# Optimization experiments

Hardware: AMD Instinct MI355X
Metric: run time of the kernel (lower is better)

The kernel has to match this reference:

```python
import jax, jax.numpy as jnp
import numpy as np

N, E, B = 16384, 131072, 256
F_IN, HID, HEADS, F_CELL, N_OUT = 78, 128, 10, 954, 2
NEG_SLOPE = 0.2  # PyG GATConv default


def setup_inputs() -> dict:
    key = jax.random.key(0)
    ks = jax.random.split(key, 24)
    rn = lambda k, shape, s=0.05: (jax.random.normal(k, shape, jnp.float32) * s)
    inp = {
        "x": rn(ks[0], (N, F_IN), 1.0),
        "edge_index": jax.random.randint(ks[1], (2, E), 0, N, dtype=jnp.int32),
        "batch": (jnp.arange(N, dtype=jnp.int32) // (N // B)),  # 64 nodes per graph, sorted
        "cell": rn(ks[2], (B, F_CELL), 1.0),
        "W1": rn(ks[3], (F_IN, HEADS * HID)),
        "a_src1": rn(ks[4], (HEADS, HID)),
        "a_dst1": rn(ks[5], (HEADS, HID)),
        "b1": jnp.zeros((HEADS * HID,), jnp.float32),
        # GATConv layer 2: 1280 -> 128, 1 head
        "W2": rn(ks[6], (HEADS * HID, HID)),
        "a_src2": rn(ks[7], (1, HID)),
        "a_dst2": rn(ks[8], (1, HID)),
        "b2": jnp.zeros((HID,), jnp.float32),
        # drug1_fc_g1: 128 -> 128
        "Wg": rn(ks[9], (HID, HID)), "bg": jnp.zeros((HID,), jnp.float32),
        # fc head applied to normalized cell (source applies fc1 to cell: 954 -> 2048)
        "Wf1": rn(ks[10], (F_CELL, 2048)), "bf1": jnp.zeros((2048,), jnp.float32),
        "Wf2": rn(ks[11], (2048, 512)), "bf2": jnp.zeros((512,), jnp.float32),
        "Wf3": rn(ks[12], (512, 128)), "bf3": jnp.zeros((128,), jnp.float32),
        "Wo": rn(ks[13], (128, N_OUT)), "bo": jnp.zeros((N_OUT,), jnp.float32),
    }
    return inp


def _gat_layer(xin, src, dst, W, a_s, a_d, b, heads, ch):
    """PyG GATConv: linear -> per-edge leaky_relu(a_src.h_j + a_dst.h_i) ->
    segment softmax over incoming edges of dst -> scatter-add of alpha * h_src."""
    n = xin.shape[0]
    h = (xin @ W).reshape(n, heads, ch)                       # [N,H,C]
    es = jnp.einsum('nhc,hc->nh', h, a_s)                     # alpha_src per node
    ed = jnp.einsum('nhc,hc->nh', h, a_d)                     # alpha_dst per node
    e = jax.nn.leaky_relu(es[src] + ed[dst], NEG_SLOPE)       # [Etot,H]
    m = jax.ops.segment_max(e, dst, num_segments=n)           # stable softmax max
    w = jnp.exp(e - m[dst])                                   # unnormalized alpha
    denom = jax.ops.segment_sum(w, dst, num_segments=n)       # [N,H]
    num = jax.ops.segment_sum(w[:, :, None] * h[src], dst, num_segments=n)  # [N,H,C]
    out = num / denom[:, :, None]
    return out.reshape(n, heads * ch) + b


def reference(x, edge_index, batch, cell, W1, a_src1, a_dst1, b1,
              W2, a_src2, a_dst2, b2, Wg, bg, Wf1, bf1, Wf2, bf2,
              Wf3, bf3, Wo, bo):
    n = x.shape[0]
    # add self-loops (PyG GATConv default)
    loop = jnp.arange(n, dtype=edge_index.dtype)
    src = jnp.concatenate([edge_index[0], loop])
    dst = jnp.concatenate([edge_index[1], loop])

    x1 = jax.nn.elu(_gat_layer(x, src, dst, W1, a_src1, a_dst1, b1, HEADS, HID))
    x1 = jax.nn.elu(_gat_layer(x1, src, dst, W2, a_src2, a_dst2, b2, 1, HID))
    # global max pool over graphs (batch is sorted, all B segments non-empty)
    x1 = jax.ops.segment_max(x1, batch, num_segments=B)       # [B,128]
    x1 = jax.nn.relu(x1 @ Wg + bg)

    # cell branch: L2 normalize rows, then dense head (dropout = identity in eval)
    celln = cell / jnp.maximum(jnp.linalg.norm(cell, axis=1, keepdims=True), 1e-12)
    xc = jax.nn.relu(celln @ Wf1 + bf1)
    xc = jax.nn.relu(xc @ Wf2 + bf2)
    xc = jax.nn.relu(xc @ Wf3 + bf3)
    out = xc @ Wo + bo                                        # [B,2]
    # source returns only `out`; we also expose the (otherwise-dead) GAT branch
    return jnp.concatenate([x1, out], axis=1)                 # [B,130]
```

## Files before the change

### kernel.cpp

```cpp
#include <hip/hip_runtime.h>
#include <hip/hip_bf16.h>
#include <math.h>

#define N_NODES 16384
#define E_EDGES 131072
#define ETOT (E_EDGES + N_NODES)
#define BGRAPH 256
#define F_INPUT 78
#define KPAD1 96
#define HID 128
#define HEADS 10
#define F1 (HEADS * HID)
#define F_CELL 954
#define KPADC 960
#define NEG_SLOPE 0.2f

typedef __attribute__((ext_vector_type(8))) short frag_t;
typedef __attribute__((ext_vector_type(4))) float f4_t;

static __device__ __forceinline__ unsigned fkey(float f) {
    unsigned b = __float_as_uint(f);
    return (b & 0x80000000u) ? ~b : (b | 0x80000000u);
}
static __device__ __forceinline__ float funkey(unsigned k) {
    unsigned b = (k & 0x80000000u) ? (k ^ 0x80000000u) : ~k;
    return __uint_as_float(b);
}
static __device__ __forceinline__ unsigned short f2bf(float f) {
    __hip_bfloat16 h = __float2bfloat16(f);
    return *(unsigned short*)&h;
}
static __device__ __forceinline__ float bf2f(unsigned short u) {
    return __uint_as_float(((unsigned)u) << 16);
}

template<int WM16, int WN16, int OUT_MODE, int ACT, int HAS_BIAS>
__global__ __launch_bounds__(256) void mfma_gemm(
    const unsigned short* __restrict__ A, const unsigned short* __restrict__ BT,
    const float* __restrict__ bias, void* __restrict__ C,
    float* __restrict__ esp, float* __restrict__ edp,
    const float* __restrict__ ca, const float* __restrict__ cd,
    int M, int N, int Kpad, int lda, int ldb, int ldc,
    int za, int zb, int zc, int zbias)
{
    constexpr int BM = 32 * WM16, BN = 32 * WN16;
    __shared__ __align__(16) unsigned short Als[BM * 32];
    __shared__ __align__(16) unsigned short Bls[BN * 32];
    const int z = blockIdx.z;
    A  += (size_t)z * za;
    BT += (size_t)z * zb;
    const int t = threadIdx.x;
    const int wave = t >> 6, lane = t & 63;
    const int wr = (wave >> 1) * (16 * WM16);
    const int wc = (wave & 1) * (16 * WN16);
    const int row0 = blockIdx.y * BM;
    const int col0 = blockIdx.x * BN;

    f4_t acc[WM16][WN16];
#pragma unroll
    for (int m = 0; m < WM16; m++)
#pragma unroll
        for (int n = 0; n < WN16; n++) { acc[m][n] = (f4_t){0.f, 0.f, 0.f, 0.f}; }

    const int lrow = lane & 15, kg = lane >> 4;
    for (int kk = 0; kk < Kpad; kk += 32) {
        for (int i = t; i < BM * 4; i += 256) {
            int r = i >> 2, slot = i & 3;
            uint4 v = *(const uint4*)&A[(size_t)(row0 + r) * lda + kk + slot * 8];
            *(uint4*)&Als[r * 32 + ((slot ^ (r & 3) ^ ((r >> 2) & 3)) * 8)] = v;
        }
        for (int i = t; i < BN * 4; i += 256) {
            int r = i >> 2, slot = i & 3;
            uint4 v = *(const uint4*)&BT[(size_t)(col0 + r) * ldb + kk + slot * 8];
            *(uint4*)&Bls[r * 32 + ((slot ^ (r & 3) ^ ((r >> 2) & 3)) * 8)] = v;
        }
        __syncthreads();
        frag_t af[WM16], bfr[WN16];
#pragma unroll
        for (int m = 0; m < WM16; m++) {
            int r = wr + m * 16 + lrow;
            af[m] = *(frag_t*)&Als[r * 32 + ((kg ^ (r & 3) ^ ((r >> 2) & 3)) * 8)];
        }
#pragma unroll
        for (int n = 0; n < WN16; n++) {
            int r = wc + n * 16 + lrow;
            bfr[n] = *(frag_t*)&Bls[r * 32 + ((kg ^ (r & 3) ^ ((r >> 2) & 3)) * 8)];
        }
#pragma unroll
        for (int m = 0; m < WM16; m++)
#pragma unroll
            for (int n = 0; n < WN16; n++)
                acc[m][n] = __builtin_amdgcn_mfma_f32_16x16x32_bf16(af[m], bfr[n], acc[m][n], 0, 0, 0);
        __syncthreads();
    }

    if constexpr (OUT_MODE <= 2 || OUT_MODE == 5) {
#pragma unroll
        for (int m = 0; m < WM16; m++) {
#pragma unroll
            for (int n = 0; n < WN16; n++) {
                int col = col0 + wc + n * 16 + lrow;
                float bv = HAS_BIAS ? bias[z * zbias + col] : 0.f;
#pragma unroll
                for (int r = 0; r < 4; r++) {
                    int row = row0 + wr + m * 16 + kg * 4 + r;
                    float v = acc[m][n][r] + bv;
                    if (ACT == 1) v = fmaxf(v, 0.f);
                    if (ACT == 2) v = (v > 0.f) ? v : expm1f(v);
                    size_t ci = (size_t)row * ldc + (size_t)z * zc + col;
                    if (OUT_MODE == 0)      ((float*)C)[ci] = v;
                    else if (OUT_MODE == 1) ((unsigned short*)C)[ci] = f2bf(v);
                    else if (OUT_MODE == 5) atomicAdd(&((float*)C)[(size_t)row * ldc + col], acc[m][n][r]);
                    else {
                        if (col < 10)                  esp[row * 10 + col] = v;
                        else if (col >= 16 && col < 26) edp[row * 10 + (col - 16)] = v;
                    }
                }
            }
        }
    } else {
        __shared__ float o2l[BM][2];
        if (t < BM) { o2l[t][0] = 0.f; o2l[t][1] = 0.f; }
        __syncthreads();
#pragma unroll
        for (int m = 0; m < WM16; m++) {
#pragma unroll
            for (int r = 0; r < 4; r++) {
                int lr = wr + m * 16 + kg * 4 + r;
                float p0 = 0.f, p1 = 0.f;
#pragma unroll
                for (int n = 0; n < WN16; n++) {
                    int col = col0 + wc + n * 16 + lrow;
                    float v = acc[m][n][r] + (HAS_BIAS ? bias[col] : 0.f);
                    if (ACT == 1) v = fmaxf(v, 0.f);
                    p0 = fmaf(v, ca[col * 2], p0);
                    p1 = fmaf(v, ca[col * 2 + 1], p1);
                }
                atomicAdd(&o2l[lr][0], p0);
                atomicAdd(&o2l[lr][1], p1);
            }
        }
        __syncthreads();
        if (t < BM) {
            ((float*)C)[(size_t)(row0 + t) * ldc + 128] = o2l[t][0] + cd[0];
            ((float*)C)[(size_t)(row0 + t) * ldc + 129] = o2l[t][1] + cd[1];
        }
    }
}

#define S0 1572864
#define S1 122880
#define S2 163840
#define S3 1966080
#define S4 1048576
#define S5 65536
#define S6 16384
#define PREP_TOTAL (S0+S1+S2+S3+S4+S5+S6)
#define NB_ELEM (PREP_TOTAL / 256)
#define NB_FOLD 768
#define NB_ZCNT 64
#define NB_ZPK  128
#define NB_ZH2F 8192

__global__ void prep_all(const float* __restrict__ x,  const float* __restrict__ W1,
                         const float* __restrict__ W2, const float* __restrict__ Wf1,
                         const float* __restrict__ Wf2, const float* __restrict__ Wf3,
                         const float* __restrict__ Wg,
                         const float* __restrict__ as1, const float* __restrict__ ad1,
                         unsigned short* __restrict__ xb,  unsigned short* __restrict__ W1T,
                         unsigned short* __restrict__ W2T, unsigned short* __restrict__ Wf1T,
                         unsigned short* __restrict__ Wf2T, unsigned short* __restrict__ Wf3T,
                         unsigned short* __restrict__ WgT, unsigned short* __restrict__ F1T,
                         int* __restrict__ counts, unsigned* __restrict__ pk,
                         float* __restrict__ H2f)
{
    int blk = blockIdx.x, t = threadIdx.x;
    if (blk < NB_ELEM) {
        int i = blk * 256 + t;
        if (i < S0) { int r = i / 96, k = i % 96;
            xb[i] = (k < F_INPUT) ? f2bf(x[r * F_INPUT + k]) : 0; return; }
        i -= S0;
        if (i < S1) { int n = i / 96, k = i % 96;
            W1T[i] = (k < F_INPUT) ? f2bf(W1[(size_t)k * F1 + n]) : 0; return; }
        i -= S1;
        if (i < S2) { int n = i / 1280, k = i % 1280;
            W2T[i] = f2bf(W2[(size_t)k * HID + n]); return; }
        i -= S2;
        if (i < S3) { int n = i / 960, k = i % 960;
            Wf1T[i] = (k < F_CELL) ? f2bf(Wf1[(size_t)k * 2048 + n]) : 0; return; }
        i -= S3;
        if (i < S4) { int n = i / 2048, k = i % 2048;
            Wf2T[i] = f2bf(Wf2[(size_t)k * 512 + n]); return; }
        i -= S4;
        if (i < S5) { int n = i / 512, k = i % 512;
            Wf3T[i] = f2bf(Wf3[(size_t)k * HID + n]); return; }
        i -= S5;
        { int n = i / 128, k = i % 128;
            WgT[i] = f2bf(Wg[(size_t)k * HID + n]); }
        return;
    }
    blk -= NB_ELEM;
    if (blk < NB_FOLD) {
        int idx = blk * 4 + (t >> 6);
        int l = t & 63;
        int r = idx / 96, k = idx % 96;
        int sd = r >> 4, h = r & 15;
        float p = 0.f;
        if (h < HEADS && k < F_INPUT) {
            const float* a = (sd ? ad1 : as1) + h * HID;
            float2 wv = *(const float2*)&W1[(size_t)k * F1 + h * HID + 2 * l];
            float2 av = *(const float2*)&a[2 * l];
            p = wv.x * av.x + wv.y * av.y;
#pragma unroll
            for (int o = 32; o > 0; o >>= 1) p += __shfl_xor(p, o);
        }
        if (l == 0) F1T[(size_t)r * 96 + k] = f2bf(p);
        return;
    }
    blk -= NB_FOLD;
    if (blk < NB_ZCNT) { counts[blk * 256 + t] = 0; return; }
    blk -= NB_ZCNT;
    if (blk < NB_ZPK) { pk[blk * 256 + t] = 0; return; }
    blk -= NB_ZPK;
    H2f[(size_t)blk * 256 + t] = 0.f;
}

__global__ void hist_dst(const int* __restrict__ ei, int* __restrict__ counts)
{
    int e = blockIdx.x * blockDim.x + threadIdx.x;
    if (e >= ETOT) return;
    int dst = (e < E_EDGES) ? ei[E_EDGES + e] : (e - E_EDGES);
    atomicAdd(&counts[dst], 1);
}

__global__ void scan_counts(const int* __restrict__ counts,
                            int* __restrict__ row_start, int* __restrict__ cursor)
{
    __shared__ int part[256];
    int t = threadIdx.x;
    int base = t * 64;
    int sum = 0;
    for (int i = 0; i < 64; i++) sum += counts[base + i];
    part[t] = sum;
    __syncthreads();
    for (int o = 1; o < 256; o <<= 1) {
        int v = 0;
        if (t >= o) v = part[t - o];
        __syncthreads();
        part[t] += v;
        __syncthreads();
    }
    int run = (t == 0) ? 0 : part[t - 1];
    for (int i = 0; i < 64; i++) {
        row_start[base + i] = run;
        cursor[base + i] = run;
        run += counts[base + i];
    }
    if (t == 255) row_start[N_NODES] = run;
}

__global__ void scatter_csr(const int* __restrict__ ei, int* __restrict__ cursor,
                            int* __restrict__ csr_src)
{
    int e = blockIdx.x * blockDim.x + threadIdx.x;
    if (e >= ETOT) return;
    int src, dst;
    if (e < E_EDGES) { src = ei[e]; dst = ei[E_EDGES + e]; } else { src = dst = e - E_EDGES; }
    int pos = atomicAdd(&cursor[dst], 1);
    csr_src[pos] = src;
}

__global__ __launch_bounds__(256) void h2_convert(
    const float* __restrict__ H2f, const float* __restrict__ as_,
    const float* __restrict__ ad_, unsigned short* __restrict__ H2,
    float* __restrict__ es, float* __restrict__ ed)
{
    int n = blockIdx.x * 4 + (threadIdx.x >> 6);
    int l = threadIdx.x & 63;
    float2 v = *(const float2*)&H2f[(size_t)n * HID + 2 * l];
    float2 av = *(const float2*)&as_[2 * l];
    float2 dv = *(const float2*)&ad_[2 * l];
    float vs = v.x * av.x + v.y * av.y;
    float vd = v.x * dv.x + v.y * dv.y;
#pragma unroll
    for (int o = 32; o > 0; o >>= 1) { vs += __shfl_xor(vs, o); vd += __shfl_xor(vd, o); }
    if (l == 0) { es[n] = vs; ed[n] = vd; }
    unsigned pw = (unsigned)f2bf(v.x) | ((unsigned)f2bf(v.y) << 16);
    *(unsigned*)&H2[(size_t)n * HID + 2 * l] = pw;
}

__global__ __launch_bounds__(256) void gat1_agg(
    const int* __restrict__ row_start, const int* __restrict__ csr_src,
    const unsigned* __restrict__ xb32,
    const float* __restrict__ es, const float* __restrict__ ed,
    unsigned* __restrict__ aggb)
{
    const int w = threadIdx.x >> 6, l = threadIdx.x & 63;
    const int n = blockIdx.x * 4 + w;
    const int rs = row_start[n];
    const int deg = row_start[n + 1] - rs;

    __shared__ __align__(16) float w_lds[4][64][12];
    __shared__ int src_lds[4][64];

    float edv[HEADS];
    const float* edp = ed + n * HEADS;
#pragma unroll
    for (int h = 0; h < HEADS; h++) edv[h] = edp[h];

    float acc0[HEADS], acc1[HEADS], den[HEADS];
#pragma unroll
    for (int h = 0; h < HEADS; h++) { acc0[h] = 0.f; acc1[h] = 0.f; den[h] = 0.f; }

    for (int base = 0; base < deg; base += 64) {
        int e = base + l;
        int cnt = min(64, deg - base);
        float wv[HEADS];
        if (e < deg) {
            int s = csr_src[rs + e];
            src_lds[w][l] = s;
            const float* ep = es + s * HEADS;
#pragma unroll
            for (int h = 0; h < HEADS; h++) {
                float v = ep[h] + edv[h];
                v = (v >= 0.f) ? v : NEG_SLOPE * v;
                wv[h] = __expf(v);
            }
        } else {
#pragma unroll
            for (int h = 0; h < HEADS; h++) wv[h] = 0.f;
        }
#pragma unroll
        for (int h = 0; h < HEADS; h++) {
            den[h] += wv[h];
            w_lds[w][l][h] = wv[h];
        }
        asm volatile("" ::: "memory");

        for (int j = 0; j < cnt; j++) {
            int sj = src_lds[w][j];
            unsigned xv = 0;
            if (l < 48) xv = xb32[(size_t)sj * 48 + l];
            float x0 = bf2f((unsigned short)(xv & 0xffffu));
            float x1v = bf2f((unsigned short)(xv >> 16));
            float4 wa = *(const float4*)&w_lds[w][j][0];
            float4 wb = *(const float4*)&w_lds[w][j][4];
            float2 wcv = *(const float2*)&w_lds[w][j][8];
            float ww[HEADS] = {wa.x, wa.y, wa.z, wa.w, wb.x, wb.y, wb.z, wb.w, wcv.x, wcv.y};
#pragma unroll
            for (int h = 0; h < HEADS; h++) {
                acc0[h] = fmaf(ww[h], x0, acc0[h]);
                acc1[h] = fmaf(ww[h], x1v, acc1[h]);
            }
        }
        asm volatile("" ::: "memory");
    }

#pragma unroll
    for (int h = 0; h < HEADS; h++)
#pragma unroll
        for (int o = 32; o > 0; o >>= 1) den[h] += __shfl_xor(den[h], o);

    if (l < 48) {
        unsigned* orow = aggb + (size_t)n * 480;
#pragma unroll
        for (int h = 0; h < HEADS; h++) {
            float inv = 1.f / den[h];
            unsigned lo = f2bf(acc0[h] * inv);
            unsigned hi = f2bf(acc1[h] * inv);
            orow[h * 48 + l] = lo | (hi << 16);
        }
    }
}

__global__ __launch_bounds__(256) void gat2_agg(
    const int* __restrict__ row_start, const int* __restrict__ csr_src,
    const unsigned short* __restrict__ H2,
    const float* __restrict__ es, const float* __restrict__ ed,
    const float* __restrict__ b, const int* __restrict__ batch,
    unsigned* __restrict__ pk)
{
    const int w = threadIdx.x >> 6, l = threadIdx.x & 63;
    const int n = blockIdx.x * 4 + w;
    const int rs = row_start[n];
    const int deg = row_start[n + 1] - rs;
    const float edv = ed[n];

    float2 acc = {0.f, 0.f};
    float den = 0.f;
    for (int base = 0; base < deg; base += 64) {
        int e = base + l;
        int cnt = min(64, deg - base);
        int s = 0;
        float wv = 0.f;
        if (e < deg) {
            s = csr_src[rs + e];
            float v = es[s] + edv;
            v = (v >= 0.f) ? v : NEG_SLOPE * v;
            wv = __expf(v);
        }
        den += wv;
        for (int j = 0; j < cnt; j++) {
            float wj = __shfl(wv, j);
            int   sj = __shfl(s, j);
            unsigned hp = *(const unsigned*)&H2[(size_t)sj * HID + 2 * l];
            acc.x = fmaf(wj, bf2f((unsigned short)(hp & 0xffffu)), acc.x);
            acc.y = fmaf(wj, bf2f((unsigned short)(hp >> 16)), acc.y);
        }
    }
#pragma unroll
    for (int o = 32; o > 0; o >>= 1) den += __shfl_xor(den, o);

    float inv = 1.f / den;
    float2 bv = *(const float2*)&b[2 * l];
    float v0 = acc.x * inv + bv.x;
    float v1 = acc.y * inv + bv.y;
    v0 = (v0 > 0.f) ? v0 : expm1f(v0);
    v1 = (v1 > 0.f) ? v1 : expm1f(v1);
    int g = batch[n];
    atomicMax(&pk[g * HID + 2 * l], fkey(v0));
    atomicMax(&pk[g * HID + 2 * l + 1], fkey(v1));
}

__global__ void decode_cell(const unsigned* __restrict__ pk,
                            unsigned short* __restrict__ pooledb,
                            const float* __restrict__ cell,
                            unsigned short* __restrict__ celln)
{
    int t = threadIdx.x;
    if (blockIdx.x < BGRAPH) {
        int b = blockIdx.x;
        __shared__ float red[256];
        float s = 0.f;
        for (int c = t; c < F_CELL; c += 256) { float v = cell[(size_t)b * F_CELL + c]; s += v * v; }
        red[t] = s; __syncthreads();
        for (int o = 128; o > 0; o >>= 1) { if (t < o) red[t] += red[t + o]; __syncthreads(); }
        float inv = 1.f / fmaxf(sqrtf(red[0]), 1e-12f);
        for (int c = t; c < KPADC; c += 256) {
            float v = (c < F_CELL) ? cell[(size_t)b * F_CELL + c] * inv : 0.f;
            celln[(size_t)b * KPADC + c] = f2bf(v);
        }
    } else {
        int i = (blockIdx.x - BGRAPH) * 256 + t;
        if (i < BGRAPH * HID) pooledb[i] = f2bf(funkey(pk[i]));
    }
}

extern "C" void kernel_launch(void* const* d_in, const int* in_sizes, int n_in,
                              void* d_out, int out_size, void* d_ws, size_t ws_size,
                              hipStream_t stream)
{
    const float* x    = (const float*)d_in[0];
    const int*   ei   = (const int*)d_in[1];
    const int*   batch= (const int*)d_in[2];
    const float* cell = (const float*)d_in[3];
    const float* W1   = (const float*)d_in[4];
    const float* as1  = (const float*)d_in[5];
    const float* ad1  = (const float*)d_in[6];
    const float* b1   = (const float*)d_in[7];
    const float* W2   = (const float*)d_in[8];
    const float* as2  = (const float*)d_in[9];
    const float* ad2  = (const float*)d_in[10];
    const float* b2   = (const float*)d_in[11];
    const float* Wg   = (const float*)d_in[12];
    const float* bg   = (const float*)d_in[13];
    const float* Wf1  = (const float*)d_in[14];
    const float* bf1  = (const float*)d_in[15];
    const float* Wf2  = (const float*)d_in[16];
    const float* bf2  = (const float*)d_in[17];
    const float* Wf3  = (const float*)d_in[18];
    const float* bf3  = (const float*)d_in[19];
    const float* Wo   = (const float*)d_in[20];
    const float* bo   = (const float*)d_in[21];
    float* out = (float*)d_out;

    char* w = (char*)d_ws;
    auto alloc = [&](size_t bytes) { char* p = w; w += (bytes + 255) & ~(size_t)255; return p; };
    unsigned short* xb   = (unsigned short*)alloc((size_t)N_NODES * KPAD1 * 2);
    unsigned short* W1T  = (unsigned short*)alloc((size_t)F1 * KPAD1 * 2);
    unsigned short* F1T  = (unsigned short*)alloc((size_t)32 * KPAD1 * 2);
    unsigned*       aggb = (unsigned*)alloc((size_t)N_NODES * 480 * 4);
    unsigned short* x1   = (unsigned short*)alloc((size_t)N_NODES * F1 * 2);
    unsigned short* W2T  = (unsigned short*)alloc((size_t)HID * F1 * 2);
    float*          H2f  = (float*)alloc((size_t)N_NODES * HID * 4);
    unsigned short* H2   = (unsigned short*)alloc((size_t)N_NODES * HID * 2);
    float*    es1  = (float*)alloc((size_t)N_NODES * HEADS * 4);
    float*    ed1  = (float*)alloc((size_t)N_NODES * HEADS * 4);
    float*    es2  = (float*)alloc((size_t)N_NODES * 4);
    float*    ed2  = (float*)alloc((size_t)N_NODES * 4);
    int*      counts    = (int*)alloc((size_t)N_NODES * 4);
    int*      row_start = (int*)alloc((size_t)(N_NODES + 1) * 4);
    int*      cursor    = (int*)alloc((size_t)N_NODES * 4);
    int*      csr_src   = (int*)alloc((size_t)ETOT * 4);
    unsigned* pk   = (unsigned*)alloc((size_t)BGRAPH * HID * 4);
    unsigned short* pooledb = (unsigned short*)alloc((size_t)BGRAPH * HID * 2);
    unsigned short* WgT  = (unsigned short*)alloc((size_t)HID * HID * 2);
    unsigned short* celln = (unsigned short*)alloc((size_t)BGRAPH * KPADC * 2);
    unsigned short* Wf1T = (unsigned short*)alloc((size_t)2048 * KPADC * 2);
    unsigned short* Wf2T = (unsigned short*)alloc((size_t)512 * 2048 * 2);
    unsigned short* Wf3T = (unsigned short*)alloc((size_t)HID * 512 * 2);
    unsigned short* xc1b = (unsigned short*)alloc((size_t)BGRAPH * 2048 * 2);
    unsigned short* xc2b = (unsigned short*)alloc((size_t)BGRAPH * 512 * 2);

    dim3 b256(256);
    const int egrid = (ETOT + 255) / 256;

    prep_all<<<NB_ELEM + NB_FOLD + NB_ZCNT + NB_ZPK + NB_ZH2F, b256, 0, stream>>>(
        x, W1, W2, Wf1, Wf2, Wf3, Wg, as1, ad1,
        xb, W1T, W2T, Wf1T, Wf2T, Wf3T, WgT, F1T, counts, pk, H2f);

    hist_dst<<<egrid, b256, 0, stream>>>(ei, counts);
    scan_counts<<<1, b256, 0, stream>>>(counts, row_start, cursor);
    scatter_csr<<<egrid, b256, 0, stream>>>(ei, cursor, csr_src);

    mfma_gemm<4, 1, 2, 0, 0><<<dim3(1, N_NODES / 128), b256, 0, stream>>>(
        xb, F1T, nullptr, nullptr, es1, ed1, nullptr, nullptr,
        N_NODES, 32, KPAD1, KPAD1, KPAD1, 32, 0, 0, 0, 0);

    gat1_agg<<<N_NODES / 4, b256, 0, stream>>>(row_start, csr_src, (const unsigned*)xb,
                                               es1, ed1, aggb);

    mfma_gemm<4, 4, 1, 2, 1><<<dim3(1, N_NODES / 128, HEADS), b256, 0, stream>>>(
        (const unsigned short*)aggb, W1T, b1, x1, nullptr, nullptr, nullptr, nullptr,
        N_NODES, HID, KPAD1, 960, KPAD1, F1, KPAD1, HID * KPAD1, HID, HID);

    mfma_gemm<2, 4, 5, 0, 0><<<dim3(1, N_NODES / 64, 4), b256, 0, stream>>>(
        x1, W2T, nullptr, H2f, nullptr, nullptr, nullptr, nullptr,
        N_NODES, HID, F1 / 4, F1, F1, HID, F1 / 4, F1 / 4, 0, 0);

    h2_convert<<<N_NODES / 4, b256, 0, stream>>>(H2f, as2, ad2, H2, es2, ed2);

    gat2_agg<<<N_NODES / 4, b256, 0, stream>>>(row_start, csr_src, H2, es2, ed2, b2,
                                               batch, pk);

    decode_cell<<<BGRAPH + (BGRAPH * HID + 255) / 256, b256, 0, stream>>>(
        pk, pooledb, cell, celln);

    mfma_gemm<2, 2, 0, 1, 1><<<dim3(HID / 64, BGRAPH / 64), b256, 0, stream>>>(
        pooledb, WgT, bg, out, nullptr, nullptr, nullptr, nullptr,
        BGRAPH, HID, HID, HID, HID, 130, 0, 0, 0, 0);

    mfma_gemm<2, 2, 1, 1, 1><<<dim3(2048 / 64, BGRAPH / 64), b256, 0, stream>>>(
        celln, Wf1T, bf1, xc1b, nullptr, nullptr, nullptr, nullptr,
        BGRAPH, 2048, KPADC, KPADC, KPADC, 2048, 0, 0, 0, 0);
    mfma_gemm<1, 2, 1, 1, 1><<<dim3(512 / 64, BGRAPH / 32), b256, 0, stream>>>(
        xc1b, Wf2T, bf2, xc2b, nullptr, nullptr, nullptr, nullptr,
        BGRAPH, 512, 2048, 2048, 2048, 512, 0, 0, 0, 0);

    mfma_gemm<2, 4, 4, 1, 1><<<dim3(1, BGRAPH / 64), b256, 0, stream>>>(
        xc2b, Wf3T, bf3, out, nullptr, nullptr, Wo, bo,
        BGRAPH, HID, 512, 512, 512, 130, 0, 0, 0, 0);
}
```

Before: 253.1 us.

## Replace split-K atomic H2 GEMM with double-buffered full-K kernel writing bf16

The layer-2 linear (16384x1280 @ 1280x128) previously used a 4-way split-K GEMM that atomically added fp32 partials into a zeroed buffer, then a separate pass converted it to bf16 and computed attention coefficients. A new dedicated kernel processes the full K with double-buffered LDS prefetching and writes bf16 output directly, so the fp32 buffer, its zeroing and the atomics go away. A lighter kernel now computes es/ed from the bf16 H2, which slightly changes precision because the dot products use rounded values. Each block covers only 32 rows across all 128 columns, giving 512 blocks with no K parallelism, which may leave the GPU less occupied than before.

```diff
diff --git a/kernel.cpp b/kernel.cpp
--- a/kernel.cpp
+++ b/kernel.cpp
@@ -94,7 +94,7 @@
         __syncthreads();
     }
 
-    if constexpr (OUT_MODE <= 2 || OUT_MODE == 5) {
+    if constexpr (OUT_MODE <= 2) {
 #pragma unroll
         for (int m = 0; m < WM16; m++) {
 #pragma unroll
@@ -110,7 +110,6 @@
                     size_t ci = (size_t)row * ldc + (size_t)z * zc + col;
                     if (OUT_MODE == 0)      ((float*)C)[ci] = v;
                     else if (OUT_MODE == 1) ((unsigned short*)C)[ci] = f2bf(v);
-                    else if (OUT_MODE == 5) atomicAdd(&((float*)C)[(size_t)row * ldc + col], acc[m][n][r]);
                     else {
                         if (col < 10)                  esp[row * 10 + col] = v;
                         else if (col >= 16 && col < 26) edp[row * 10 + (col - 16)] = v;
@@ -144,6 +143,83 @@
         if (t < BM) {
             ((float*)C)[(size_t)(row0 + t) * ldc + 128] = o2l[t][0] + cd[0];
             ((float*)C)[(size_t)(row0 + t) * ldc + 129] = o2l[t][1] + cd[1];
+        }
+    }
+}
+
+__global__ __launch_bounds__(256) void h2_gemm(
+    const unsigned short* __restrict__ A, const unsigned short* __restrict__ BT,
+    unsigned short* __restrict__ C)
+{
+    __shared__ __align__(16) unsigned short Als[2][32 * 32];
+    __shared__ __align__(16) unsigned short Bls[2][128 * 32];
+    const int t = threadIdx.x;
+    const int wave = t >> 6, lane = t & 63;
+    const int lrow = lane & 15, kg = lane >> 4;
+    const int row0 = blockIdx.x * 32;
+    const int wc = wave * 32;
+
+    const int ar = t >> 2, asl = t & 3;
+    const int br = t >> 2, bsl = t & 3;
+
+    uint4 pa, pb0, pb1;
+    auto LOAD = [&](int kk) {
+        if (t < 128) pa = *(const uint4*)&A[(size_t)(row0 + ar) * F1 + kk + asl * 8];
+        pb0 = *(const uint4*)&BT[(size_t)br * F1 + kk + bsl * 8];
+        pb1 = *(const uint4*)&BT[(size_t)(br + 64) * F1 + kk + bsl * 8];
+    };
+    auto STORE = [&](int buf) {
+        if (t < 128)
+            *(uint4*)&Als[buf][ar * 32 + ((asl ^ (ar & 3) ^ ((ar >> 2) & 3)) * 8)] = pa;
+        *(uint4*)&Bls[buf][br * 32 + ((bsl ^ (br & 3) ^ ((br >> 2) & 3)) * 8)] = pb0;
+        int r2 = br + 64;
+        *(uint4*)&Bls[buf][r2 * 32 + ((bsl ^ (r2 & 3) ^ ((r2 >> 2) & 3)) * 8)] = pb1;
+    };
+
+    LOAD(0);
+    STORE(0);
+    __syncthreads();
+
+    f4_t acc[2][2];
+#pragma unroll
+    for (int m = 0; m < 2; m++)
+#pragma unroll
+        for (int n = 0; n < 2; n++) acc[m][n] = (f4_t){0.f, 0.f, 0.f, 0.f};
+
+    int cur = 0;
+    for (int ks = 0; ks < 40; ks++) {
+        if (ks < 39) LOAD((ks + 1) * 32);
+        frag_t af[2], bfr[2];
+#pragma unroll
+        for (int m = 0; m < 2; m++) {
+            int r = m * 16 + lrow;
+            af[m] = *(frag_t*)&Als[cur][r * 32 + ((kg ^ (r & 3) ^ ((r >> 2) & 3)) * 8)];
+        }
+#pragma unroll
+        for (int n = 0; n < 2; n++) {
+            int r = wc + n * 16 + lrow;
+            bfr[n] = *(frag_t*)&Bls[cur][r * 32 + ((kg ^ (r & 3) ^ ((r >> 2) & 3)) * 8)];
+        }
+#pragma unroll
+        for (int m = 0; m < 2; m++)
+#pragma unroll
+            for (int n = 0; n < 2; n++)
+                acc[m][n] = __builtin_amdgcn_mfma_f32_16x16x32_bf16(af[m], bfr[n], acc[m][n], 0, 0, 0);
+        if (ks < 39) STORE(cur ^ 1);
+        __syncthreads();
+        cur ^= 1;
+    }
+
+#pragma unroll
+    for (int m = 0; m < 2; m++) {
+#pragma unroll
+        for (int n = 0; n < 2; n++) {
+            int col = wc + n * 16 + lrow;
+#pragma unroll
+            for (int r = 0; r < 4; r++) {
+                int row = row0 + m * 16 + kg * 4 + r;
+                C[(size_t)row * HID + col] = f2bf(acc[m][n][r]);
+            }
         }
     }
 }
@@ -160,7 +236,6 @@
 #define NB_FOLD 768
 #define NB_ZCNT 64
 #define NB_ZPK  128
-#define NB_ZH2F 8192
 
 __global__ void prep_all(const float* __restrict__ x,  const float* __restrict__ W1,
                          const float* __restrict__ W2, const float* __restrict__ Wf1,
@@ -171,8 +246,7 @@
                          unsigned short* __restrict__ W2T, unsigned short* __restrict__ Wf1T,
                          unsigned short* __restrict__ Wf2T, unsigned short* __restrict__ Wf3T,
                          unsigned short* __restrict__ WgT, unsigned short* __restrict__ F1T,
-                         int* __restrict__ counts, unsigned* __restrict__ pk,
-                         float* __restrict__ H2f)
+                         int* __restrict__ counts, unsigned* __restrict__ pk)
 {
     int blk = blockIdx.x, t = threadIdx.x;
     if (blk < NB_ELEM) {
@@ -220,9 +294,7 @@
     blk -= NB_FOLD;
     if (blk < NB_ZCNT) { counts[blk * 256 + t] = 0; return; }
     blk -= NB_ZCNT;
-    if (blk < NB_ZPK) { pk[blk * 256 + t] = 0; return; }
-    blk -= NB_ZPK;
-    H2f[(size_t)blk * 256 + t] = 0.f;
+    pk[blk * 256 + t] = 0;
 }
 
 __global__ void hist_dst(const int* __restrict__ ei, int* __restrict__ counts)
@@ -270,23 +342,22 @@
     csr_src[pos] = src;
 }
 
-__global__ __launch_bounds__(256) void h2_convert(
-    const float* __restrict__ H2f, const float* __restrict__ as_,
-    const float* __restrict__ ad_, unsigned short* __restrict__ H2,
-    float* __restrict__ es, float* __restrict__ ed)
+__global__ void h2_coef(const unsigned short* __restrict__ H2,
+                        const float* __restrict__ as_, const float* __restrict__ ad_,
+                        float* __restrict__ es, float* __restrict__ ed)
 {
     int n = blockIdx.x * 4 + (threadIdx.x >> 6);
     int l = threadIdx.x & 63;
-    float2 v = *(const float2*)&H2f[(size_t)n * HID + 2 * l];
+    unsigned p = *(const unsigned*)&H2[(size_t)n * HID + 2 * l];
+    float h0 = bf2f((unsigned short)(p & 0xffffu));
+    float h1 = bf2f((unsigned short)(p >> 16));
     float2 av = *(const float2*)&as_[2 * l];
     float2 dv = *(const float2*)&ad_[2 * l];
-    float vs = v.x * av.x + v.y * av.y;
-    float vd = v.x * dv.x + v.y * dv.y;
+    float vs = h0 * av.x + h1 * av.y;
+    float vd = h0 * dv.x + h1 * dv.y;
 #pragma unroll
     for (int o = 32; o > 0; o >>= 1) { vs += __shfl_xor(vs, o); vd += __shfl_xor(vd, o); }
     if (l == 0) { es[n] = vs; ed[n] = vd; }
-    unsigned pw = (unsigned)f2bf(v.x) | ((unsigned)f2bf(v.y) << 16);
-    *(unsigned*)&H2[(size_t)n * HID + 2 * l] = pw;
 }
 
 __global__ __launch_bounds__(256) void gat1_agg(
@@ -482,7 +553,6 @@
     unsigned*       aggb = (unsigned*)alloc((size_t)N_NODES * 480 * 4);
     unsigned short* x1   = (unsigned short*)alloc((size_t)N_NODES * F1 * 2);
     unsigned short* W2T  = (unsigned short*)alloc((size_t)HID * F1 * 2);
-    float*          H2f  = (float*)alloc((size_t)N_NODES * HID * 4);
     unsigned short* H2   = (unsigned short*)alloc((size_t)N_NODES * HID * 2);
     float*    es1  = (float*)alloc((size_t)N_NODES * HEADS * 4);
     float*    ed1  = (float*)alloc((size_t)N_NODES * HEADS * 4);
@@ -505,9 +575,9 @@
     dim3 b256(256);
     const int egrid = (ETOT + 255) / 256;
 
-    prep_all<<<NB_ELEM + NB_FOLD + NB_ZCNT + NB_ZPK + NB_ZH2F, b256, 0, stream>>>(
+    prep_all<<<NB_ELEM + NB_FOLD + NB_ZCNT + NB_ZPK, b256, 0, stream>>>(
         x, W1, W2, Wf1, Wf2, Wf3, Wg, as1, ad1,
-        xb, W1T, W2T, Wf1T, Wf2T, Wf3T, WgT, F1T, counts, pk, H2f);
+        xb, W1T, W2T, Wf1T, Wf2T, Wf3T, WgT, F1T, counts, pk);
 
     hist_dst<<<egrid, b256, 0, stream>>>(ei, counts);
     scan_counts<<<1, b256, 0, stream>>>(counts, row_start, cursor);
@@ -524,11 +594,9 @@
         (const unsigned short*)aggb, W1T, b1, x1, nullptr, nullptr, nullptr, nullptr,
         N_NODES, HID, KPAD1, 960, KPAD1, F1, KPAD1, HID * KPAD1, HID, HID);
 
-    mfma_gemm<2, 4, 5, 0, 0><<<dim3(1, N_NODES / 64, 4), b256, 0, stream>>>(
-        x1, W2T, nullptr, H2f, nullptr, nullptr, nullptr, nullptr,
-        N_NODES, HID, F1 / 4, F1, F1, HID, F1 / 4, F1 / 4, 0, 0);
-
-    h2_convert<<<N_NODES / 4, b256, 0, stream>>>(H2f, as2, ad2, H2, es2, ed2);
+    h2_gemm<<<N_NODES / 32, b256, 0, stream>>>(x1, W2T, H2);
+
+    h2_coef<<<N_NODES / 4, b256, 0, stream>>>(H2, as2, ad2, es2, ed2);
 
     gat2_agg<<<N_NODES / 4, b256, 0, stream>>>(row_start, csr_src, H2, es2, ed2, b2,
                                                batch, pk);
```

Result: faster. 232.1 us (-8.3%).
